# Kernel optimization log

Measured on AMD Instinct MI355X. Metric: run time of the kernel, lower is better.

Reference implementation:

```python
import jax, jax.numpy as jnp
import numpy as np

L, H, D, DFF, B, S = 4, 8, 512, 2048, 2, 2048
DH = D // H
EPS = 1e-5
SCALE_BASE = 512.0


def setup_inputs() -> dict:
    key = jax.random.key(0)
    ks = jax.random.split(key, 8)
    def w(k, shape, s=0.02):
        return jax.random.normal(k, shape, jnp.float32) * s
    return {
        "x": jax.random.normal(ks[0], (B, S, D), jnp.float32),
        "WQ": w(ks[1], (L, H, D, DH)),
        "WK": w(ks[2], (L, H, D, DH)),
        "WV": w(ks[3], (L, H, D, DH)),
        "WG": w(ks[4], (L, D, D)),
        "WO": w(ks[5], (L, D, D)),
        "gn_w": jnp.ones((L, D), jnp.float32),
        "gn_b": jnp.zeros((L, D), jnp.float32),
        "ln1_w": jnp.ones((L, D), jnp.float32),
        "ln1_b": jnp.zeros((L, D), jnp.float32),
        "ln2_w": jnp.ones((L, D), jnp.float32),
        "ln2_b": jnp.zeros((L, D), jnp.float32),
        "ffn_w1": w(ks[6], (L, D, DFF)),
        "ffn_b1": jnp.zeros((L, DFF), jnp.float32),
        "ffn_w2": w(ks[7], (L, DFF, D)),
        "ffn_b2": jnp.zeros((L, D), jnp.float32),
    }


def _dup(t):
    # duplicate_interleave: [a,b] -> [a,a,b,b]
    return jnp.repeat(t, 2, axis=-1)


def _rot(x):
    # rotate_every_two: (x1,x2) -> (-x2, x1)
    x1, x2 = x[..., ::2], x[..., 1::2]
    return jnp.stack([-x2, x1], axis=-1).reshape(x.shape)


def _xpos(x, downscale):
    # x: [B,H,S,dh]  XPOS rotary with length-extrapolating scale
    s_len, dh = x.shape[-2], x.shape[-1]
    half = dh // 2
    base = (jnp.arange(0, dh, 2, dtype=jnp.float32) + 0.4 * dh) / (1.4 * dh)  # [half]
    power = jnp.arange(s_len, dtype=jnp.float32) / SCALE_BASE
    scale = base[None, :] ** power[:, None]  # [S, half]
    if downscale:
        scale = 1.0 / scale
    inv_freq = 1.0 / (10000.0 ** (jnp.arange(half, dtype=jnp.float32) / half))
    ang = jnp.arange(s_len, dtype=jnp.float32)[:, None] * inv_freq[None, :]
    sin, cos, sc = _dup(jnp.sin(ang)), _dup(jnp.cos(ang)), _dup(scale)
    return x * cos * sc + _rot(x) * sin * sc


def _ln(x, w, b):
    mu = jnp.mean(x, -1, keepdims=True)
    var = jnp.mean((x - mu) ** 2, -1, keepdims=True)
    return (x - mu) * jax.lax.rsqrt(var + EPS) * w + b


def reference(x, WQ, WK, WV, WG, WO, gn_w, gn_b, ln1_w, ln1_b, ln2_w, ln2_b, ffn_w1, ffn_b1, ffn_w2, ffn_b2):
    gammas = 1.0 - jnp.exp(jnp.linspace(np.log(1.0 / 32.0), np.log(1.0 / 512.0), H)).astype(jnp.float32)
    idx = jnp.arange(S, dtype=jnp.float32)
    diff = idx[:, None] - idx[None, :]
    Dmask = jnp.where(diff >= 0, gammas[:, None, None] ** diff, 0.0)  # [H,S,S]
    b = x.shape[0]
    for i in range(L):
        xn = _ln(x, ln1_w[i], ln1_b[i])
        q = _xpos(jnp.einsum('bsd,hde->bhse', xn, WQ[i]), False)
        k = _xpos(jnp.einsum('bsd,hde->bhse', xn, WK[i]), True)
        v = jnp.einsum('bsd,hde->bhse', xn, WV[i])
        att = jnp.einsum('bhse,bhte->bhst', q, k) * Dmask[None]  # [B,H,S,S]
        yh = jnp.einsum('bhst,bhte->bhse', att, v)               # [B,H,S,dh]
        yh = yh.transpose(0, 2, 1, 3)                            # [B,S,H,dh]
        mu = jnp.mean(yh, -1, keepdims=True)
        var = jnp.mean((yh - mu) ** 2, -1, keepdims=True)
        yn = (yh - mu) * jax.lax.rsqrt(var + EPS)
        yn = yn * gn_w[i].reshape(H, DH) + gn_b[i].reshape(H, DH)
        y = yn.reshape(b, S, D)
        g = jax.nn.silu(xn @ WG[i])
        y1 = (g * y) @ WO[i] + x
        h = _ln(y1, ln2_w[i], ln2_b[i])
        x = jax.nn.gelu(h @ ffn_w1[i] + ffn_b1[i], approximate=False) @ ffn_w2[i] + ffn_b2[i] + y1
    return x
```

## Files before the change

kernel.cpp:

```cpp
#include <hip/hip_runtime.h>
#include <hip/hip_bf16.h>

#define LYR 4
#define NH  8
#define DM  512
#define DHD 64
#define DFF 2048
#define BB  2
#define SSL 2048
#define NROWS (BB*SSL)

typedef unsigned short u16;
typedef __attribute__((ext_vector_type(8))) short bf16x8;
typedef __attribute__((ext_vector_type(4))) float f32x4;
typedef __attribute__((ext_vector_type(4))) unsigned int u32x4;

__device__ __forceinline__ u16 f2bf(float f) {
    union { float f; unsigned u; } v; v.f = f;
    unsigned r = v.u + 0x7FFFu + ((v.u >> 16) & 1u);
    return (u16)(r >> 16);
}
__device__ __forceinline__ float bf2f(u16 b) {
    union { unsigned u; float f; } v; v.u = ((unsigned)b) << 16;
    return v.f;
}
__device__ __forceinline__ int swz(int row, int col) {
    return row * 64 + (col & 7) + ((((col >> 3) ^ row) & 7) << 3);
}
__device__ __forceinline__ int swzP(int row, int col) {
    return row * 128 + (col & 7) + ((((col >> 3) ^ row) & 15) << 3);
}
__device__ __forceinline__ void gload16(const u16* g, u16* l) {
    __builtin_amdgcn_global_load_lds(
        (const __attribute__((address_space(1))) unsigned int*)g,
        (__attribute__((address_space(3))) unsigned int*)l, 16, 0, 0);
}
template <int N> __device__ __forceinline__ void wait_vmcnt() {
    if constexpr (N == 0)      asm volatile("s_waitcnt vmcnt(0)" ::: "memory");
    else if constexpr (N == 6) asm volatile("s_waitcnt vmcnt(6)" ::: "memory");
    else static_assert(N == 0 || N == 6, "unsupported vmcnt");
}
__device__ __forceinline__ void block_barrier() {
    __builtin_amdgcn_s_barrier();
    asm volatile("" ::: "memory");
}


__global__ __launch_bounds__(256) void xpos_tables(float4* __restrict__ tab4) {
    const int idx = blockIdx.x * 256 + threadIdx.x;
    const int s = idx >> 5, j = idx & 31;
    const float base = (2.f * j + 0.4f * 64.f) / (1.4f * 64.f);
    const float invf = powf(10000.f, -(float)j / 32.f);
    const float ang = (float)s * invf;
    const float scq = powf(base, (float)s / 512.f);
    tab4[idx] = make_float4(sinf(ang), cosf(ang), scq, 1.f / scq);
}

__global__ __launch_bounds__(256)
void prep_qkv(const float* __restrict__ WQp, const float* __restrict__ WKp,
              const float* __restrict__ WVp, u16* __restrict__ WBT) {
    const int dt = blockIdx.x;
    const int h = blockIdx.y & 7, which = blockIdx.y >> 3;
    const int l = blockIdx.z;
    const float* W = (which == 0 ? WQp : which == 1 ? WKp : WVp);
    const float* ip = W + ((size_t)(l * 8 + h)) * (512 * 64);
    u16* op = WBT + (size_t)l * (2048 * 512) + (size_t)(which * 512 + h * 64) * 512;
    __shared__ u16 tile[64 * 72];
    const int t = threadIdx.x, rr = t >> 2, cc = (t & 3) * 16;
    const float* src = ip + (size_t)(dt * 64 + rr) * 64 + cc;
#pragma unroll
    for (int i = 0; i < 16; ++i) tile[rr * 72 + cc + i] = f2bf(src[i]);
    __syncthreads();
    u16 tmp[16] __attribute__((aligned(16)));
#pragma unroll
    for (int i = 0; i < 16; ++i) tmp[i] = tile[(cc + i) * 72 + rr];
    u16* dst = op + (size_t)rr * 512 + dt * 64 + cc;
    *(u32x4*)&dst[0] = *(const u32x4*)&tmp[0];
    *(u32x4*)&dst[8] = *(const u32x4*)&tmp[8];
}

__global__ __launch_bounds__(256)
void prep_t(const float* __restrict__ in, u16* __restrict__ out, int R, int C,
            long long in_ls, long long out_ls) {
    const float* ip = in + (size_t)blockIdx.z * in_ls;
    u16* op = out + (size_t)blockIdx.z * out_ls;
    const int r0 = blockIdx.x * 64, c0t = blockIdx.y * 64;
    __shared__ u16 tile[64 * 72];
    const int t = threadIdx.x, rr = t >> 2, cc = (t & 3) * 16;
    const float* src = ip + (size_t)(r0 + rr) * C + c0t + cc;
#pragma unroll
    for (int i = 0; i < 16; ++i) tile[rr * 72 + cc + i] = f2bf(src[i]);
    __syncthreads();
    u16 tmp[16] __attribute__((aligned(16)));
#pragma unroll
    for (int i = 0; i < 16; ++i) tmp[i] = tile[(cc + i) * 72 + rr];
    u16* dst = op + (size_t)(c0t + rr) * R + r0 + cc;
    *(u32x4*)&dst[0] = *(const u32x4*)&tmp[0];
    *(u32x4*)&dst[8] = *(const u32x4*)&tmp[8];
}

__global__ __launch_bounds__(256)
void ln_kernel(const float* __restrict__ x, const float* __restrict__ wt,
               const float* __restrict__ bs, u16* __restrict__ out) {
    const int row = blockIdx.x * 4 + (threadIdx.x >> 6);
    const int lane = threadIdx.x & 63;
    const float* xr = x + (size_t)row * DM + lane * 8;
    float v[8];
    *(float4*)&v[0] = *(const float4*)&xr[0];
    *(float4*)&v[4] = *(const float4*)&xr[4];
    float s = 0.f, s2 = 0.f;
#pragma unroll
    for (int i = 0; i < 8; ++i) { s += v[i]; s2 += v[i] * v[i]; }
#pragma unroll
    for (int m = 1; m < 64; m <<= 1) {
        s  += __shfl_xor(s, m, 64);
        s2 += __shfl_xor(s2, m, 64);
    }
    const float mu = s * (1.f / DM);
    const float rs = rsqrtf(s2 * (1.f / DM) - mu * mu + 1e-5f);
    const int e0 = lane * 8;
    u16 o[8] __attribute__((aligned(16)));
#pragma unroll
    for (int i = 0; i < 8; ++i)
        o[i] = f2bf((v[i] - mu) * rs * wt[e0 + i] + bs[e0 + i]);
    *(u32x4*)&out[(size_t)row * DM + e0] = *(const u32x4*)o;
}

template <int BM, int BN, int EPI>
__global__ __launch_bounds__(256)
void gemm_bt(const u16* __restrict__ A, const u16* __restrict__ Bt,
             u16* __restrict__ obf, float* __restrict__ of32,
             const float* __restrict__ res, const float* __restrict__ bias,
             int M, int N, int K) {
    constexpr int FM = BM / 32, FN = BN / 32;
    constexpr int LPS = BM / 32 + BN / 32;
    static_assert(LPS == 6, "vmcnt template expects 6");
    __shared__ __align__(16) u16 As[2][BM * 64];
    __shared__ __align__(16) u16 Bs[2][BN * 64];
    const int t = threadIdx.x;
    const int lane = t & 63, w4 = t >> 6;
    const int wr = w4 >> 1, wc = w4 & 1;
    const int fr = lane & 15, fq = lane >> 4;
    const int nX = N / BN;
    const int nwg = (M / BM) * nX;
    const int swzid = (blockIdx.x & 7) * (nwg >> 3) + (blockIdx.x >> 3);
    const int m0 = (swzid / nX) * BM, n0 = (swzid % nX) * BN;
    const int lr = lane >> 3;
    const int ls = lane & 7;
    const int nsteps = K >> 6;

    auto stage = [&](int step, int slot) {
        const int k0 = step << 6;
#pragma unroll
        for (int q = 0; q < BM / 32; ++q) {
            const int ib = q * 4 + w4;
            const int row = ib * 8 + lr;
            const int cc = ls ^ (row & 7);
            gload16(&A[(size_t)(m0 + row) * K + k0 + cc * 8], &As[slot][ib * 512]);
        }
#pragma unroll
        for (int q = 0; q < BN / 32; ++q) {
            const int ib = q * 4 + w4;
            const int row = ib * 8 + lr;
            const int cc = ls ^ (row & 7);
            gload16(&Bt[(size_t)(n0 + row) * K + k0 + cc * 8], &Bs[slot][ib * 512]);
        }
    };

    f32x4 acc[FM][FN] = {};
    stage(0, 0);
    stage(1, 1);
    for (int st = 0; st < nsteps; ++st) {
        if (st + 1 < nsteps) wait_vmcnt<LPS>(); else wait_vmcnt<0>();
        __builtin_amdgcn_sched_barrier(0);
        block_barrier();
        const u16* Ac = As[st & 1];
        const u16* Bc = Bs[st & 1];
#pragma unroll
        for (int ks = 0; ks < 2; ++ks) {
            bf16x8 av[FM], bv[FN];
#pragma unroll
            for (int i = 0; i < FM; ++i)
                av[i] = *(const bf16x8*)&Ac[swz(wr * (BM / 2) + i * 16 + fr, ks * 32 + fq * 8)];
#pragma unroll
            for (int j = 0; j < FN; ++j)
                bv[j] = *(const bf16x8*)&Bc[swz(wc * (BN / 2) + j * 16 + fr, ks * 32 + fq * 8)];
#pragma unroll
            for (int i = 0; i < FM; ++i)
#pragma unroll
                for (int j = 0; j < FN; ++j)
                    acc[i][j] = __builtin_amdgcn_mfma_f32_16x16x32_bf16(av[i], bv[j], acc[i][j], 0, 0, 0);
        }
        asm volatile("s_waitcnt lgkmcnt(0)" ::: "memory");
        __builtin_amdgcn_sched_barrier(0);
        block_barrier();
        if (st + 2 < nsteps) stage(st + 2, st & 1);
    }
#pragma unroll
    for (int i = 0; i < FM; ++i)
#pragma unroll
        for (int j = 0; j < FN; ++j)
#pragma unroll
            for (int r = 0; r < 4; ++r) {
                const int m = m0 + wr * (BM / 2) + i * 16 + fq * 4 + r;
                const int n = n0 + wc * (BN / 2) + j * 16 + fr;
                const size_t idx = (size_t)m * N + n;
                float v = acc[i][j][r];
                if constexpr (EPI == 1) {
                    of32[idx] = v + res[idx];
                } else {
                    of32[idx] = v + bias[n] + res[idx];
                }
            }
}

template <int EPI>
__global__ __launch_bounds__(512, 1)
void gemm_big(const u16* __restrict__ A, const u16* __restrict__ Bt,
              u16* __restrict__ obf, const float* __restrict__ bias,
              u16* __restrict__ qb, u16* __restrict__ kb, u16* __restrict__ vt,
              u16* __restrict__ gb, const float4* __restrict__ tab4,
              int M, int N, int K) {
    constexpr int BM = 256, BN = 128;
    __shared__ __align__(16) u16 SM[49152];
    const int t = threadIdx.x;
    const int lane = t & 63, w = t >> 6;
    const int wr = w >> 2, wcn = w & 3;
    const int fr = lane & 15, fq = lane >> 4;
    const int nX = N / BN;
    const int nwg = (M / BM) * nX;
    const int swzid = (blockIdx.x & 7) * (nwg >> 3) + (blockIdx.x >> 3);
    const int m0 = (swzid / nX) * BM, n0 = (swzid % nX) * BN;
    const int lr = lane >> 3, ls = lane & 7;
    const int nsteps = K >> 6;

    auto stage = [&](int step, int slot) {
        const int k0 = step << 6;
#pragma unroll
        for (int q = 0; q < 4; ++q) {
            const int ib = q * 8 + w;
            const int row = ib * 8 + lr;
            const int cc = ls ^ (row & 7);
            gload16(&A[(size_t)(m0 + row) * K + k0 + cc * 8], &SM[slot * 16384 + ib * 512]);
        }
#pragma unroll
        for (int q = 0; q < 2; ++q) {
            const int ib = q * 8 + w;
            const int row = ib * 8 + lr;
            const int cc = ls ^ (row & 7);
            gload16(&Bt[(size_t)(n0 + row) * K + k0 + cc * 8],
                    &SM[32768 + slot * 8192 + ib * 512]);
        }
    };

    f32x4 acc[8][2] = {};
    stage(0, 0);
    stage(1, 1);
    for (int st = 0; st < nsteps; ++st) {
        if (st + 1 < nsteps) wait_vmcnt<6>(); else wait_vmcnt<0>();
        __builtin_amdgcn_sched_barrier(0);
        block_barrier();
        const u16* Ac = &SM[(st & 1) * 16384];
        const u16* Bc = &SM[32768 + (st & 1) * 8192];
#pragma unroll
        for (int ks = 0; ks < 2; ++ks) {
            bf16x8 bv[2];
#pragma unroll
            for (int j = 0; j < 2; ++j)
                bv[j] = *(const bf16x8*)&Bc[swz(wcn * 32 + j * 16 + fr, ks * 32 + fq * 8)];
            __builtin_amdgcn_s_setprio(1);
#pragma unroll
            for (int i = 0; i < 8; ++i) {
                bf16x8 av = *(const bf16x8*)&Ac[swz(wr * 128 + i * 16 + fr, ks * 32 + fq * 8)];
                acc[i][0] = __builtin_amdgcn_mfma_f32_16x16x32_bf16(av, bv[0], acc[i][0], 0, 0, 0);
                acc[i][1] = __builtin_amdgcn_mfma_f32_16x16x32_bf16(av, bv[1], acc[i][1], 0, 0, 0);
            }
            __builtin_amdgcn_s_setprio(0);
        }
        asm volatile("s_waitcnt lgkmcnt(0)" ::: "memory");
        __builtin_amdgcn_sched_barrier(0);
        block_barrier();
        if (st + 2 < nsteps) stage(st + 2, st & 1);
    }

    if constexpr (EPI == 2) {
#pragma unroll
        for (int i = 0; i < 8; ++i)
#pragma unroll
            for (int j = 0; j < 2; ++j)
#pragma unroll
                for (int r = 0; r < 4; ++r) {
                    const int m = m0 + wr * 128 + i * 16 + fq * 4 + r;
                    const int n = n0 + wcn * 32 + j * 16 + fr;
                    float tt = acc[i][j][r] + bias[n];
                    obf[(size_t)m * N + n] = f2bf(0.5f * tt * (1.f + erff(tt * 0.7071067811865475f)));
                }
    } else {
        const int region = n0 >> 9;
        const int h = (n0 & 511) >> 6;
        const int b = m0 >> 11;
        const int s0 = m0 & 2047;
        if (region == 3) {
#pragma unroll
            for (int i = 0; i < 8; ++i)
#pragma unroll
                for (int j = 0; j < 2; ++j)
#pragma unroll
                    for (int r = 0; r < 4; ++r) {
                        const int m = m0 + wr * 128 + i * 16 + fq * 4 + r;
                        const int el = wcn * 32 + j * 16 + fr;
                        gb[(size_t)m * 512 + (n0 & 511) + el] = f2bf(acc[i][j][r]);
                    }
        } else if (region <= 1) {
            u16* dst = (region == 0) ? qb : kb;
#pragma unroll
            for (int i = 0; i < 8; ++i)
#pragma unroll
                for (int j = 0; j < 2; ++j)
#pragma unroll
                    for (int r = 0; r < 4; ++r) {
                        const int s = s0 + wr * 128 + i * 16 + fq * 4 + r;
                        const int el = wcn * 32 + j * 16 + fr;
                        const int hh = h + (el >> 6), e = el & 63;
                        const float v = acc[i][j][r];
                        const float p = __shfl_xor(v, 1, 64);
                        const float rot = (e & 1) ? p : -p;
                        const float4 t4 = tab4[(size_t)s * 32 + (e >> 1)];
                        const float scl = (region == 0) ? t4.z : t4.w;
                        dst[((size_t)(b * NH + hh) * 2048 + s) * 64 + e] =
                            f2bf((v * t4.y + rot * t4.x) * scl);
                    }
        } else {
            u16* LT = SM;
#pragma unroll
            for (int i = 0; i < 8; ++i)
#pragma unroll
                for (int j = 0; j < 2; ++j)
#pragma unroll
                    for (int r = 0; r < 4; ++r) {
                        const int sl = wr * 128 + i * 16 + fq * 4 + r;
                        const int el = wcn * 32 + j * 16 + fr;
                        LT[el * 264 + sl] = f2bf(acc[i][j][r]);
                    }
            __syncthreads();
            for (int c = t; c < 128 * 32; c += 512) {
                const int er = c >> 5;
                const int sc = (c & 31) * 8;
                const int hh = h + (er >> 6), e = er & 63;
                *(u32x4*)&vt[((size_t)(b * NH + hh) * 64 + e) * 2048 + s0 + sc] =
                    *(const u32x4*)&LT[er * 264 + sc];
            }
        }
    }
}

__global__ __launch_bounds__(512)
void retention(const u16* __restrict__ Qb, const u16* __restrict__ Kb,
               const u16* __restrict__ Vt, const u16* __restrict__ gate,
               const float* __restrict__ gnw, const float* __restrict__ gnb,
               u16* __restrict__ zb) {
    extern __shared__ __align__(16) char smem[];
    u16* KsB = (u16*)smem;
    u16* VsB = (u16*)(smem + 32768);
    u16* Qs  = (u16*)(smem + 65536);
    u16* Ps  = (u16*)(smem + 73728);

    const int logical = (blockIdx.x & 7) * 64 + (blockIdx.x >> 3);
    const int bh = logical >> 5;
    const int qt = 31 - (logical & 31);
    const int h = bh & 7, b = bh >> 3;
    const int t = threadIdx.x;
    const int lane = t & 63, w = t >> 6;
    const int fr = lane & 15, fq = lane >> 4;
    const int wr = w & 1, wc2 = w >> 1;
    const int oc = wc2 & 1, th = w >> 2;

    const float gamma = 1.f - expf(-3.4657359f + (float)h * -0.39608410f);
    const float lgam = log2f(gamma);
    const float dlim = 19.931568f / (-lgam);
    const int jt_last = (qt * 64 + 63) >> 7;
    int jt_min = 0;
    {
        const float need = (float)(qt * 64 - 127) - dlim;
        if (need > 0.f) jt_min = (int)ceilf(need * (1.f / 128.f));
        if (jt_min > jt_last) jt_min = jt_last;
        if (jt_min < 0) jt_min = 0;
    }

    float rowf[2][4], colf[2];
#pragma unroll
    for (int i = 0; i < 2; ++i)
#pragma unroll
        for (int rr = 0; rr < 4; ++rr)
            rowf[i][rr] = exp2f((float)(wr * 32 + i * 16 + fq * 4 + rr) * lgam);
#pragma unroll
    for (int j = 0; j < 2; ++j)
        colf[j] = exp2f(-(float)(wc2 * 32 + j * 16 + fr) * lgam);

    const size_t bh2048 = (size_t)bh * 2048;
    const int lr8 = lane >> 3, ls8 = lane & 7;
    const int lr16 = lane >> 4, ls16 = lane & 15;

    {
        const int row = w * 8 + lr8;
        const int cc = ls8 ^ (row & 7);
        gload16(&Qb[(bh2048 + qt * 64 + row) * 64 + cc * 8], &Qs[w * 512]);
    }

    f32x4 oacc[2][2] = {};
    int cur = 0;
    {
        const int jt = jt_min;
        u16* Kd = KsB; u16* Vd = VsB;
#pragma unroll
        for (int q = 0; q < 2; ++q) {
            const int row = q * 64 + w * 8 + lr8;
            const int cc = ls8 ^ (row & 7);
            gload16(&Kb[(bh2048 + jt * 128 + row) * 64 + cc * 8], &Kd[(q * 64 + w * 8) * 64]);
        }
#pragma unroll
        for (int q = 0; q < 2; ++q) {
            const int row = w * 8 + q * 4 + lr16;
            const int cc = ls16 ^ (row & 15);
            gload16(&Vt[((size_t)bh * 64 + row) * 2048 + jt * 128 + cc * 8], &Vd[(w * 8 + q * 4) * 128]);
        }
    }

    for (int jt = jt_min; jt <= jt_last; ++jt) {
        __syncthreads();
        if (jt < jt_last) {
            const int nb = cur ^ 1;
            u16* Kd = KsB + nb * 8192;
            u16* Vd = VsB + nb * 8192;
#pragma unroll
            for (int q = 0; q < 2; ++q) {
                const int row = q * 64 + w * 8 + lr8;
                const int cc = ls8 ^ (row & 7);
                gload16(&Kb[(bh2048 + (jt + 1) * 128 + row) * 64 + cc * 8], &Kd[(q * 64 + w * 8) * 64]);
            }
#pragma unroll
            for (int q = 0; q < 2; ++q) {
                const int row = w * 8 + q * 4 + lr16;
                const int cc = ls16 ^ (row & 15);
                gload16(&Vt[((size_t)bh * 64 + row) * 2048 + (jt + 1) * 128 + cc * 8], &Vd[(w * 8 + q * 4) * 128]);
            }
        }
        const u16* Kc = KsB + cur * 8192;
        f32x4 sac[2][2] = {};
#pragma unroll
        for (int ks = 0; ks < 2; ++ks) {
            bf16x8 qa[2], kb2[2];
#pragma unroll
            for (int i = 0; i < 2; ++i)
                qa[i] = *(const bf16x8*)&Qs[swz(wr * 32 + i * 16 + fr, ks * 32 + fq * 8)];
#pragma unroll
            for (int j = 0; j < 2; ++j)
                kb2[j] = *(const bf16x8*)&Kc[swz(wc2 * 32 + j * 16 + fr, ks * 32 + fq * 8)];
#pragma unroll
            for (int i = 0; i < 2; ++i)
#pragma unroll
                for (int j = 0; j < 2; ++j)
                    sac[i][j] = __builtin_amdgcn_mfma_f32_16x16x32_bf16(qa[i], kb2[j], sac[i][j], 0, 0, 0);
        }
        const float sc = exp2f((float)(qt * 64 - jt * 128) * lgam);
        const bool diag = (jt == jt_last);
#pragma unroll
        for (int i = 0; i < 2; ++i)
#pragma unroll
            for (int j = 0; j < 2; ++j)
#pragma unroll
                for (int rr = 0; rr < 4; ++rr) {
                    float m = sc * rowf[i][rr] * colf[j];
                    if (diag) {
                        const int d = (qt * 64 + wr * 32 + i * 16 + fq * 4 + rr)
                                    - (jt * 128 + wc2 * 32 + j * 16 + fr);
                        if (d < 0) m = 0.f;
                    }
                    Ps[swzP(wr * 32 + i * 16 + fq * 4 + rr, wc2 * 32 + j * 16 + fr)] =
                        f2bf(sac[i][j][rr] * m);
                }
        __syncthreads();
        const u16* Vc = VsB + cur * 8192;
#pragma unroll
        for (int ks = 0; ks < 2; ++ks) {
            const int tcol = th * 64 + ks * 32 + fq * 8;
            bf16x8 pa[2], vb[2];
#pragma unroll
            for (int i = 0; i < 2; ++i)
                pa[i] = *(const bf16x8*)&Ps[swzP(wr * 32 + i * 16 + fr, tcol)];
#pragma unroll
            for (int j = 0; j < 2; ++j)
                vb[j] = *(const bf16x8*)&Vc[swzP(oc * 32 + j * 16 + fr, tcol)];
#pragma unroll
            for (int i = 0; i < 2; ++i)
#pragma unroll
                for (int j = 0; j < 2; ++j)
                    oacc[i][j] = __builtin_amdgcn_mfma_f32_16x16x32_bf16(pa[i], vb[j], oacc[i][j], 0, 0, 0);
        }
        cur ^= 1;
    }

    __syncthreads();
    float* Of = (float*)smem;
    if (th == 1) {
#pragma unroll
        for (int i = 0; i < 2; ++i)
#pragma unroll
            for (int j = 0; j < 2; ++j)
#pragma unroll
                for (int rr = 0; rr < 4; ++rr)
                    Of[(wr * 32 + i * 16 + fq * 4 + rr) * 66 + oc * 32 + j * 16 + fr] = oacc[i][j][rr];
    }
    __syncthreads();
    if (th == 0) {
#pragma unroll
        for (int i = 0; i < 2; ++i)
#pragma unroll
            for (int j = 0; j < 2; ++j)
#pragma unroll
                for (int rr = 0; rr < 4; ++rr) {
                    const int idx = (wr * 32 + i * 16 + fq * 4 + rr) * 66 + oc * 32 + j * 16 + fr;
                    Of[idx] += oacc[i][j][rr];
                }
    }
    __syncthreads();
    const int row = t >> 3, c0 = (t & 7) * 8;
    float v[8];
    float s = 0.f, s2 = 0.f;
#pragma unroll
    for (int i = 0; i < 8; ++i) {
        v[i] = Of[row * 66 + c0 + i];
        s += v[i]; s2 += v[i] * v[i];
    }
    s  += __shfl_xor(s, 1, 64);  s  += __shfl_xor(s, 2, 64);  s  += __shfl_xor(s, 4, 64);
    s2 += __shfl_xor(s2, 1, 64); s2 += __shfl_xor(s2, 2, 64); s2 += __shfl_xor(s2, 4, 64);
    const float mu = s * (1.f / 64.f);
    const float rs = rsqrtf(s2 * (1.f / 64.f) - mu * mu + 1e-5f);
    const int sg = qt * 64 + row;
    u16 gv[8] __attribute__((aligned(16)));
    *(u32x4*)gv = *(const u32x4*)&gate[((size_t)(b * SSL + sg)) * 512 + h * 64 + c0];
    u16 ob[8] __attribute__((aligned(16)));
#pragma unroll
    for (int i = 0; i < 8; ++i) {
        const int dc = h * 64 + c0 + i;
        const float yn = (v[i] - mu) * rs * gnw[dc] + gnb[dc];
        const float g = bf2f(gv[i]);
        ob[i] = f2bf(yn * (g / (1.f + expf(-g))));
    }
    *(u32x4*)&zb[((size_t)(b * SSL + sg)) * 512 + h * 64 + c0] = *(const u32x4*)ob;
}

extern "C" void kernel_launch(void* const* d_in, const int* in_sizes, int n_in,
                              void* d_out, int out_size, void* d_ws, size_t ws_size,
                              hipStream_t stream) {
    const float* X    = (const float*)d_in[0];
    const float* WQ   = (const float*)d_in[1];
    const float* WK   = (const float*)d_in[2];
    const float* WV   = (const float*)d_in[3];
    const float* WG   = (const float*)d_in[4];
    const float* WO   = (const float*)d_in[5];
    const float* GNW  = (const float*)d_in[6];
    const float* GNB  = (const float*)d_in[7];
    const float* LN1W = (const float*)d_in[8];
    const float* LN1B = (const float*)d_in[9];
    const float* LN2W = (const float*)d_in[10];
    const float* LN2B = (const float*)d_in[11];
    const float* FW1  = (const float*)d_in[12];
    const float* FB1  = (const float*)d_in[13];
    const float* FW2  = (const float*)d_in[14];
    const float* FB2  = (const float*)d_in[15];

    char* ws = (char*)d_ws;
    size_t off = 0;
    auto alloc = [&](size_t n) { char* p = ws + off; off += (n + 255) & ~(size_t)255; return p; };

    u16*   WBT  = (u16*)alloc((size_t)LYR * 2048 * 512 * 2);
    u16*   WOT  = (u16*)alloc((size_t)LYR * 512 * 512 * 2);
    u16*   W1T  = (u16*)alloc((size_t)LYR * 2048 * 512 * 2);
    u16*   W2T  = (u16*)alloc((size_t)LYR * 512 * 2048 * 2);
    float4* TAB4 = (float4*)alloc((size_t)2048 * 32 * 16);
    float* XB   = (float*)alloc((size_t)NROWS * DM * 4);
    u16*   XN   = (u16*)alloc((size_t)NROWS * DM * 2);
    u16*   FF1  = (u16*)alloc((size_t)NROWS * 2048 * 2);
    u16*   GB   = (u16*)alloc((size_t)NROWS * DM * 2);
    u16*   QBp  = (u16*)alloc((size_t)NROWS * DM * 2);
    u16*   KBp  = (u16*)alloc((size_t)NROWS * DM * 2);
    u16*   VTp  = (u16*)alloc((size_t)NROWS * DM * 2);
    u16*   ZB   = (u16*)alloc((size_t)NROWS * DM * 2);
    float* Y1   = (float*)alloc((size_t)NROWS * DM * 4);
    u16*   HB   = QBp;

    xpos_tables<<<256, 256, 0, stream>>>(TAB4);
    prep_qkv<<<dim3(8, 24, LYR), 256, 0, stream>>>(WQ, WK, WV, WBT);
    prep_t<<<dim3(8, 8, LYR), 256, 0, stream>>>(WG, WBT + 1536 * 512, 512, 512,
                                                (long long)512 * 512, (long long)2048 * 512);
    prep_t<<<dim3(8, 8, LYR), 256, 0, stream>>>(WO, WOT, 512, 512,
                                                (long long)512 * 512, (long long)512 * 512);
    prep_t<<<dim3(8, 32, LYR), 256, 0, stream>>>(FW1, W1T, 512, 2048,
                                                 (long long)512 * 2048, (long long)2048 * 512);
    prep_t<<<dim3(32, 8, LYR), 256, 0, stream>>>(FW2, W2T, 2048, 512,
                                                 (long long)2048 * 512, (long long)512 * 2048);

    for (int l = 0; l < LYR; ++l) {
        const float* xsrc = (l == 0) ? X : XB;
        float* xdst = (l == LYR - 1) ? (float*)d_out : XB;
        ln_kernel<<<NROWS / 4, 256, 0, stream>>>(xsrc, LN1W + l * 512, LN1B + l * 512, XN);
        gemm_big<4><<<256, 512, 0, stream>>>(
            XN, WBT + (size_t)l * 2048 * 512, nullptr, nullptr,
            QBp, KBp, VTp, GB, TAB4, NROWS, 2048, 512);
        retention<<<512, 512, 90112, stream>>>(QBp, KBp, VTp, GB,
                                               GNW + l * 512, GNB + l * 512, ZB);
        gemm_bt<64, 128, 1><<<256, 256, 0, stream>>>(
            ZB, WOT + (size_t)l * 512 * 512, nullptr, Y1, xsrc, nullptr, NROWS, 512, 512);
        ln_kernel<<<NROWS / 4, 256, 0, stream>>>(Y1, LN2W + l * 512, LN2B + l * 512, HB);
        gemm_big<2><<<256, 512, 0, stream>>>(
            HB, W1T + (size_t)l * 2048 * 512, FF1, FB1 + l * 2048,
            nullptr, nullptr, nullptr, nullptr, nullptr, NROWS, 2048, 512);
        gemm_bt<64, 128, 3><<<256, 256, 0, stream>>>(
            FF1, W2T + (size_t)l * 512 * 2048, nullptr, xdst, Y1, FB2 + l * 512, NROWS, 512, 2048);
    }
}
```

Before: 455.9 us.

## Use 4x4 wave tiles in big GEMM and keep retention Q in registers

The big GEMM's 8 waves move from a 2x4 grid of 128x32 tiles to a 4x2 grid of 64x64 tiles. Each wave now loads 8 LDS fragments per k-step instead of 10 for the same 16 MFMAs, at the cost of more live A fragments in registers. The retention kernel reads its Q fragments straight from global memory into registers once, which removes the Q shared-memory buffer and the repeated LDS reads and shrinks dynamic LDS. It also alternates the query-tile order between heads, which changes how the causal workload is spread across blocks.

```diff
diff --git a/kernel.cpp b/kernel.cpp
--- a/kernel.cpp
+++ b/kernel.cpp
@@ -225,7 +225,7 @@
     __shared__ __align__(16) u16 SM[49152];
     const int t = threadIdx.x;
     const int lane = t & 63, w = t >> 6;
-    const int wr = w >> 2, wcn = w & 3;
+    const int wr4 = w >> 1, wc2 = w & 1;
     const int fr = lane & 15, fq = lane >> 4;
     const int nX = N / BN;
     const int nwg = (M / BM) * nX;
@@ -253,7 +253,7 @@
         }
     };
 
-    f32x4 acc[8][2] = {};
+    f32x4 acc[4][4] = {};
     stage(0, 0);
     stage(1, 1);
     for (int st = 0; st < nsteps; ++st) {
@@ -264,17 +264,19 @@
         const u16* Bc = &SM[32768 + (st & 1) * 8192];
 #pragma unroll
         for (int ks = 0; ks < 2; ++ks) {
-            bf16x8 bv[2];
-#pragma unroll
-            for (int j = 0; j < 2; ++j)
-                bv[j] = *(const bf16x8*)&Bc[swz(wcn * 32 + j * 16 + fr, ks * 32 + fq * 8)];
+            bf16x8 av[4], bv[4];
+#pragma unroll
+            for (int i = 0; i < 4; ++i)
+                av[i] = *(const bf16x8*)&Ac[swz(wr4 * 64 + i * 16 + fr, ks * 32 + fq * 8)];
+#pragma unroll
+            for (int j = 0; j < 4; ++j)
+                bv[j] = *(const bf16x8*)&Bc[swz(wc2 * 64 + j * 16 + fr, ks * 32 + fq * 8)];
             __builtin_amdgcn_s_setprio(1);
 #pragma unroll
-            for (int i = 0; i < 8; ++i) {
-                bf16x8 av = *(const bf16x8*)&Ac[swz(wr * 128 + i * 16 + fr, ks * 32 + fq * 8)];
-                acc[i][0] = __builtin_amdgcn_mfma_f32_16x16x32_bf16(av, bv[0], acc[i][0], 0, 0, 0);
-                acc[i][1] = __builtin_amdgcn_mfma_f32_16x16x32_bf16(av, bv[1], acc[i][1], 0, 0, 0);
-            }
+            for (int i = 0; i < 4; ++i)
+#pragma unroll
+                for (int j = 0; j < 4; ++j)
+                    acc[i][j] = __builtin_amdgcn_mfma_f32_16x16x32_bf16(av[i], bv[j], acc[i][j], 0, 0, 0);
             __builtin_amdgcn_s_setprio(0);
         }
         asm volatile("s_waitcnt lgkmcnt(0)" ::: "memory");
@@ -285,13 +287,13 @@
 
     if constexpr (EPI == 2) {
 #pragma unroll
-        for (int i = 0; i < 8; ++i)
-#pragma unroll
-            for (int j = 0; j < 2; ++j)
+        for (int i = 0; i < 4; ++i)
+#pragma unroll
+            for (int j = 0; j < 4; ++j)
 #pragma unroll
                 for (int r = 0; r < 4; ++r) {
-                    const int m = m0 + wr * 128 + i * 16 + fq * 4 + r;
-                    const int n = n0 + wcn * 32 + j * 16 + fr;
+                    const int m = m0 + wr4 * 64 + i * 16 + fq * 4 + r;
+                    const int n = n0 + wc2 * 64 + j * 16 + fr;
                     float tt = acc[i][j][r] + bias[n];
                     obf[(size_t)m * N + n] = f2bf(0.5f * tt * (1.f + erff(tt * 0.7071067811865475f)));
                 }
@@ -302,25 +304,25 @@
         const int s0 = m0 & 2047;
         if (region == 3) {
 #pragma unroll
-            for (int i = 0; i < 8; ++i)
-#pragma unroll
-                for (int j = 0; j < 2; ++j)
+            for (int i = 0; i < 4; ++i)
+#pragma unroll
+                for (int j = 0; j < 4; ++j)
 #pragma unroll
                     for (int r = 0; r < 4; ++r) {
-                        const int m = m0 + wr * 128 + i * 16 + fq * 4 + r;
-                        const int el = wcn * 32 + j * 16 + fr;
+                        const int m = m0 + wr4 * 64 + i * 16 + fq * 4 + r;
+                        const int el = wc2 * 64 + j * 16 + fr;
                         gb[(size_t)m * 512 + (n0 & 511) + el] = f2bf(acc[i][j][r]);
                     }
         } else if (region <= 1) {
             u16* dst = (region == 0) ? qb : kb;
 #pragma unroll
-            for (int i = 0; i < 8; ++i)
-#pragma unroll
-                for (int j = 0; j < 2; ++j)
+            for (int i = 0; i < 4; ++i)
+#pragma unroll
+                for (int j = 0; j < 4; ++j)
 #pragma unroll
                     for (int r = 0; r < 4; ++r) {
-                        const int s = s0 + wr * 128 + i * 16 + fq * 4 + r;
-                        const int el = wcn * 32 + j * 16 + fr;
+                        const int s = s0 + wr4 * 64 + i * 16 + fq * 4 + r;
+                        const int el = wc2 * 64 + j * 16 + fr;
                         const int hh = h + (el >> 6), e = el & 63;
                         const float v = acc[i][j][r];
                         const float p = __shfl_xor(v, 1, 64);
@@ -333,13 +335,13 @@
         } else {
             u16* LT = SM;
 #pragma unroll
-            for (int i = 0; i < 8; ++i)
-#pragma unroll
-                for (int j = 0; j < 2; ++j)
+            for (int i = 0; i < 4; ++i)
+#pragma unroll
+                for (int j = 0; j < 4; ++j)
 #pragma unroll
                     for (int r = 0; r < 4; ++r) {
-                        const int sl = wr * 128 + i * 16 + fq * 4 + r;
-                        const int el = wcn * 32 + j * 16 + fr;
+                        const int sl = wr4 * 64 + i * 16 + fq * 4 + r;
+                        const int el = wc2 * 64 + j * 16 + fr;
                         LT[el * 264 + sl] = f2bf(acc[i][j][r]);
                     }
             __syncthreads();
@@ -362,12 +364,12 @@
     extern __shared__ __align__(16) char smem[];
     u16* KsB = (u16*)smem;
     u16* VsB = (u16*)(smem + 32768);
-    u16* Qs  = (u16*)(smem + 65536);
-    u16* Ps  = (u16*)(smem + 73728);
+    u16* Ps  = (u16*)(smem + 65536);
 
     const int logical = (blockIdx.x & 7) * 64 + (blockIdx.x >> 3);
     const int bh = logical >> 5;
-    const int qt = 31 - (logical & 31);
+    const int u = logical & 31;
+    const int qt = (bh & 1) ? (31 - u) : u;
     const int h = bh & 7, b = bh >> 3;
     const int t = threadIdx.x;
     const int lane = t & 63, w = t >> 6;
@@ -401,11 +403,13 @@
     const int lr8 = lane >> 3, ls8 = lane & 7;
     const int lr16 = lane >> 4, ls16 = lane & 15;
 
-    {
-        const int row = w * 8 + lr8;
-        const int cc = ls8 ^ (row & 7);
-        gload16(&Qb[(bh2048 + qt * 64 + row) * 64 + cc * 8], &Qs[w * 512]);
-    }
+    bf16x8 qreg[2][2];
+#pragma unroll
+    for (int i = 0; i < 2; ++i)
+#pragma unroll
+        for (int ks = 0; ks < 2; ++ks)
+            qreg[i][ks] = *(const bf16x8*)&Qb[(bh2048 + qt * 64 + wr * 32 + i * 16 + fr) * 64
+                                             + ks * 32 + fq * 8];
 
     f32x4 oacc[2][2] = {};
     int cur = 0;
@@ -449,10 +453,7 @@
         f32x4 sac[2][2] = {};
 #pragma unroll
         for (int ks = 0; ks < 2; ++ks) {
-            bf16x8 qa[2], kb2[2];
-#pragma unroll
-            for (int i = 0; i < 2; ++i)
-                qa[i] = *(const bf16x8*)&Qs[swz(wr * 32 + i * 16 + fr, ks * 32 + fq * 8)];
+            bf16x8 kb2[2];
 #pragma unroll
             for (int j = 0; j < 2; ++j)
                 kb2[j] = *(const bf16x8*)&Kc[swz(wc2 * 32 + j * 16 + fr, ks * 32 + fq * 8)];
@@ -460,7 +461,7 @@
             for (int i = 0; i < 2; ++i)
 #pragma unroll
                 for (int j = 0; j < 2; ++j)
-                    sac[i][j] = __builtin_amdgcn_mfma_f32_16x16x32_bf16(qa[i], kb2[j], sac[i][j], 0, 0, 0);
+                    sac[i][j] = __builtin_amdgcn_mfma_f32_16x16x32_bf16(qreg[i][ks], kb2[j], sac[i][j], 0, 0, 0);
         }
         const float sc = exp2f((float)(qt * 64 - jt * 128) * lgam);
         const bool diag = (jt == jt_last);
@@ -608,7 +609,7 @@
         gemm_big<4><<<256, 512, 0, stream>>>(
             XN, WBT + (size_t)l * 2048 * 512, nullptr, nullptr,
             QBp, KBp, VTp, GB, TAB4, NROWS, 2048, 512);
-        retention<<<512, 512, 90112, stream>>>(QBp, KBp, VTp, GB,
+        retention<<<512, 512, 81920, stream>>>(QBp, KBp, VTp, GB,
                                                GNW + l * 512, GNB + l * 512, ZB);
         gemm_bt<64, 128, 1><<<256, 256, 0, stream>>>(
             ZB, WOT + (size_t)l * 512 * 512, nullptr, Y1, xsrc, nullptr, NROWS, 512, 512);
```

Result: no change. 461.4 us (+1.2%).
